# Performance work log

Hardware: AMD Instinct MI355X
Metric: run time of the kernel (lower is better)

The kernel has to match this reference:

```python
import jax, jax.numpy as jnp
import numpy as np
from jax import lax

NPOINT = 1024
RADIUS = 0.2
NSAMPLE = 32
MLP = (64, 64, 128)
BN_EPS = 1e-3  # keras BatchNormalization default epsilon


def setup_inputs() -> dict:
    key = jax.random.key(0)
    ks = jax.random.split(key, 8)
    B, N, C = 8, 8192, 64
    d = {
        'xyz': jax.random.uniform(ks[0], (B, N, 3), jnp.float32),
        'points': jax.random.normal(ks[1], (B, N, C), jnp.float32),
    }
    cin = C + 3  # use_xyz=True concatenates relative xyz
    for li, f in enumerate(MLP):
        d[f'w{li}'] = jax.random.normal(ks[2 + li], (cin, f), jnp.float32) * (1.0 / np.sqrt(cin))
        d[f'gamma{li}'] = jnp.ones((f,), jnp.float32)
        d[f'beta{li}'] = jnp.zeros((f,), jnp.float32)
        cin = f
    return d


def _fps(xyz, npoint):
    """Farthest point sampling. xyz: (B,N,3) -> (B,npoint) int32."""
    B, N, _ = xyz.shape

    def body(carry, _):
        dist, far = carry
        centroid = jnp.take_along_axis(xyz, far[:, None, None], axis=1)  # (B,1,3)
        d = jnp.sum((xyz - centroid) ** 2, axis=-1)  # (B,N)
        dist = jnp.minimum(dist, d)
        nxt = jnp.argmax(dist, axis=-1).astype(jnp.int32)
        return (dist, nxt), far

    init = (jnp.full((B, N), 1e10, xyz.dtype), jnp.zeros((B,), jnp.int32))
    _, idx = lax.scan(body, init, None, length=npoint)
    return jnp.transpose(idx)  # (B, npoint)


def _ball_query(xyz, new_xyz, radius, nsample):
    """xyz: (B,N,3), new_xyz: (B,S,3) -> (B,S,nsample) int32 neighbor idx."""
    B, S, _ = new_xyz.shape
    N = xyz.shape[1]
    sqr = jnp.sum((new_xyz[:, :, None, :] - xyz[:, None, :, :]) ** 2, axis=-1)  # (B,S,N)
    idx = jnp.broadcast_to(jnp.arange(N, dtype=jnp.int32), (B, S, N))
    idx = jnp.where(sqr > radius * radius, N, idx)
    idx = jnp.sort(idx, axis=-1)[:, :, :nsample]
    first = idx[:, :, :1]  # center itself is always in-radius -> valid
    return jnp.where(idx == N, first, idx)


def _gather(x, idx):
    """x: (B,N,C), idx: (B,S,K) -> (B,S,K,C)."""
    B, S, K = idx.shape
    flat = jnp.take_along_axis(x, idx.reshape(B, S * K)[:, :, None], axis=1)
    return flat.reshape(B, S, K, x.shape[-1])


def _bn_relu(x, gamma, beta):
    # training-mode batchnorm over (batch, npoint, nsample) axes
    m = jnp.mean(x, axis=(0, 1, 2), keepdims=True)
    v = jnp.var(x, axis=(0, 1, 2), keepdims=True)
    return jax.nn.relu(gamma * (x - m) * lax.rsqrt(v + BN_EPS) + beta)


def reference(xyz, points, w0, gamma0, beta0, w1, gamma1, beta1, w2, gamma2, beta2):
    fps_idx = _fps(xyz, NPOINT)  # (B,S)
    new_xyz = jnp.take_along_axis(xyz, fps_idx[:, :, None], axis=1)  # (B,S,3)
    idx = _ball_query(xyz, new_xyz, RADIUS, NSAMPLE)  # (B,S,K)
    grouped_xyz = _gather(xyz, idx) - new_xyz[:, :, None, :]  # (B,S,K,3)
    grouped_pts = _gather(points, idx)  # (B,S,K,C)
    x = jnp.concatenate([grouped_xyz, grouped_pts], axis=-1)  # (B,S,K,3+C)
    for w, g, b in ((w0, gamma0, beta0), (w1, gamma1, beta1), (w2, gamma2, beta2)):
        x = _bn_relu(jnp.einsum('bskc,cf->bskf', x, w), g, b)
    new_points = jnp.max(x, axis=2)  # (B,S,F) == squeeze of keepdims max
    return new_xyz, new_points
```

## Files before the change

### kernel.cpp

```cpp
#include <hip/hip_runtime.h>
#include <hip/hip_bf16.h>
#include <stdint.h>


#define INV_CNT (1.0f/262144.0f)

typedef __attribute__((ext_vector_type(8))) short bf16x8;
typedef __attribute__((ext_vector_type(4))) float f32x4;

__device__ __forceinline__ float bf2f(unsigned int v) {
    return __uint_as_float(v << 16);
}
__device__ __forceinline__ unsigned int f2bf(float f) {
    unsigned int u = __float_as_uint(f);
    return (u + 0x7fffu + ((u >> 16) & 1u)) >> 16;
}

template<int CTRL>
__device__ __forceinline__ unsigned int dpp_u32(unsigned int x) {
    return (unsigned int)__builtin_amdgcn_update_dpp((int)x, (int)x, CTRL, 0xf, 0xf, false);
}
template<int CTRL>
__device__ __forceinline__ float dpp_f32(float x) {
    return __uint_as_float(dpp_u32<CTRL>(__float_as_uint(x)));
}

__device__ __forceinline__ float2 fmin2(float2 a, float2 b) {
    return make_float2(fminf(a.x, b.x), fminf(a.y, b.y));
}
__device__ __forceinline__ float2 fmax2(float2 a, float2 b) {
    return make_float2(fmaxf(a.x, b.x), fmaxf(a.y, b.y));
}

__global__ __launch_bounds__(512) void fps_kernel(const float* __restrict__ xyz,
                                                  float* __restrict__ nxyz,
                                                  float* __restrict__ out_nxyz) {
#pragma clang fp contract(off)
    const int b = blockIdx.x;
    const int t = threadIdx.x;
    const int lane = t & 63;
    const int wv = t >> 6;
    const float* xb = xyz + (size_t)b * 8192 * 3;
    __shared__ float sx[8192], sy[8192], sz[8192];
    __shared__ unsigned long long sdk[2][8];
    __shared__ int ch[1024];
    float2 px[8], py[8], pz[8], dist[8];
#pragma unroll
    for (int j = 0; j < 8; ++j) {
        int p0 = t + (2*j)*512, p1 = t + (2*j+1)*512;
        float x0 = xb[p0*3+0], y0 = xb[p0*3+1], z0 = xb[p0*3+2];
        float x1 = xb[p1*3+0], y1 = xb[p1*3+1], z1 = xb[p1*3+2];
        px[j] = make_float2(x0, x1); py[j] = make_float2(y0, y1); pz[j] = make_float2(z0, z1);
        sx[p0] = x0; sy[p0] = y0; sz[p0] = z0;
        sx[p1] = x1; sy[p1] = y1; sz[p1] = z1;
        dist[j] = make_float2(1e10f, 1e10f);
    }
    __syncthreads();
    int far = 0;
    for (int it = 0; it < 1024; ++it) {
        if (t == 0) ch[it] = far;
        float cx = sx[far], cy = sy[far], cz = sz[far];
        float2 c2x = make_float2(cx, cx), c2y = make_float2(cy, cy), c2z = make_float2(cz, cz);
        float2 mx2 = make_float2(-1.f, -1.f);
#pragma unroll
        for (int j = 0; j < 8; ++j) {
            float2 dx = px[j] - c2x;
            float2 dy = py[j] - c2y;
            float2 dz = pz[j] - c2z;
            float2 d = (dx*dx + dy*dy) + dz*dz;
            float2 nd = fmin2(dist[j], d);
            dist[j] = nd;
            mx2 = fmax2(mx2, nd);
        }
        float v = fmaxf(mx2.x, mx2.y);
        v = fmaxf(v, dpp_f32<0x111>(v));
        v = fmaxf(v, dpp_f32<0x112>(v));
        v = fmaxf(v, dpp_f32<0x114>(v));
        v = fmaxf(v, dpp_f32<0x118>(v));
        v = fmaxf(v, dpp_f32<0x142>(v));
        v = fmaxf(v, dpp_f32<0x143>(v));
        float wm = __uint_as_float((unsigned int)__builtin_amdgcn_readlane((int)__float_as_uint(v), 63));
        unsigned int ci = 64u;
#pragma unroll
        for (int j = 7; j >= 0; --j) {
            if (dist[j].y == wm) ci = (unsigned int)(2*j+1);
            if (dist[j].x == wm) ci = (unsigned int)(2*j);
        }
        unsigned int idx = (ci == 64u) ? 0xffffffffu : (unsigned int)t + (ci << 9);
        { unsigned int n;
          n = dpp_u32<0x111>(idx); idx = (n < idx) ? n : idx;
          n = dpp_u32<0x112>(idx); idx = (n < idx) ? n : idx;
          n = dpp_u32<0x114>(idx); idx = (n < idx) ? n : idx;
          n = dpp_u32<0x118>(idx); idx = (n < idx) ? n : idx;
          n = dpp_u32<0x142>(idx); idx = (n < idx) ? n : idx;
          n = dpp_u32<0x143>(idx); idx = (n < idx) ? n : idx; }
        if (lane == 63)
            sdk[it & 1][wv] = ((unsigned long long)__float_as_uint(v) << 32)
                            | (unsigned long long)(~idx);
        __syncthreads();
        unsigned long long k = sdk[it & 1][lane & 7];
        unsigned int xh = (unsigned int)(k >> 32), xl = (unsigned int)k;
#define XSTEP(C) { unsigned int nh = dpp_u32<C>(xh), nl = dpp_u32<C>(xl);          \
                   unsigned long long nk = ((unsigned long long)nh << 32) | nl;     \
                   unsigned long long ck = ((unsigned long long)xh << 32) | xl;     \
                   bool tk = nk > ck; xh = tk ? nh : xh; xl = tk ? nl : xl; }
        XSTEP(0x111) XSTEP(0x112) XSTEP(0x114)
#undef XSTEP
        far = (int)(~(unsigned int)__builtin_amdgcn_readlane((int)xl, 7)) & 8191;
    }
    __syncthreads();
    for (int j = t; j < 1024; j += 512) {
        int ci = ch[j];
        float x = sx[ci], y = sy[ci], z = sz[ci];
        size_t o = (size_t)(b*1024 + j) * 3;
        nxyz[o] = x; nxyz[o+1] = y; nxyz[o+2] = z;
        out_nxyz[o] = x; out_nxyz[o+1] = y; out_nxyz[o+2] = z;
    }
}

__global__ __launch_bounds__(256) void ballquery_kernel(const float* __restrict__ xyz,
                                                        const float* __restrict__ nxyz,
                                                        int* __restrict__ idxbuf) {
    const int wib = threadIdx.x >> 6;
    const int lane = threadIdx.x & 63;
    const int c = blockIdx.x * 4 + wib;
    const int b = c >> 10;
    const float* xb = xyz + (size_t)b * 8192 * 3;
    const float cx = nxyz[c*3+0], cy = nxyz[c*3+1], cz = nxyz[c*3+2];
    const float R2 = 0.04f;
    int count = 0, first = 0;
    int* ob = idxbuf + (size_t)c * 32;
    for (int base = 0; base < 8192; base += 64) {
        int i = base + lane;
        float dx = __fsub_rn(xb[i*3+0], cx);
        float dy = __fsub_rn(xb[i*3+1], cy);
        float dz = __fsub_rn(xb[i*3+2], cz);
        float sq = __fadd_rn(__fadd_rn(__fmul_rn(dx,dx), __fmul_rn(dy,dy)), __fmul_rn(dz,dz));
        bool pass = !(sq > R2);
        unsigned long long mask = __ballot(pass);
        if (count == 0 && mask) first = base + (int)__builtin_ctzll(mask);
        int pos = count + (int)__popcll(mask & ((1ull << lane) - 1ull));
        if (pass && pos < 32) ob[pos] = i;
        count += (int)__popcll(mask);
        if (count >= 32) break;
    }
    if (count < 32 && lane >= count && lane < 32) ob[lane] = first;
}


__global__ __launch_bounds__(256) void layer0_kernel(
        const float* __restrict__ xyz, const float* __restrict__ points,
        const float* __restrict__ nxyz, const int* __restrict__ idxbuf,
        const float* __restrict__ w0, unsigned short* __restrict__ z0,
        float* __restrict__ stats0) {
    __shared__ __attribute__((aligned(16))) unsigned short Xb[64*104];
    __shared__ __attribute__((aligned(16))) unsigned short Wt[64*104];
    __shared__ float ssum[64], ssq[64];
    const int tid = threadIdx.x;
    const int R = blockIdx.x * 64;
    if (tid < 64) { ssum[tid] = 0.f; ssq[tid] = 0.f; }
    for (int i = tid; i < 67*64; i += 256) {
        int k = i >> 6, f = i & 63;
        Wt[f*104 + k] = (unsigned short)f2bf(w0[i]);
    }
    for (int i = tid; i < 29*64; i += 256) {
        int k = 67 + (i % 29), f = i / 29;
        Wt[f*104 + k] = 0;
    }
    {
        int r = tid >> 2, q = tid & 3;
        int row = R + r;
        int gi = idxbuf[row];
        int b = row >> 15, s = (row >> 5) & 1023;
        const float* pb = points + (size_t)(b*8192 + gi) * 64;
        int e0 = q*17, e1 = (q == 3) ? 67 : e0 + 17;
        for (int e = e0; e < e1; ++e) {
            float v;
            if (e < 3) v = xyz[(size_t)(b*8192+gi)*3 + e] - nxyz[(size_t)(b*1024+s)*3 + e];
            else       v = pb[e-3];
            Xb[r*104 + e] = (unsigned short)f2bf(v);
        }
    }
    for (int i = tid; i < 29*64; i += 256) {
        int e = 67 + (i % 29), r = i / 29;
        Xb[r*104 + e] = 0;
    }
    __syncthreads();
    const int l = tid & 63, w = tid >> 6;
    const int rsub = l & 15, kq = l >> 4;
    f32x4 acc[4];
#pragma unroll
    for (int cb = 0; cb < 4; ++cb) acc[cb] = (f32x4){0.f, 0.f, 0.f, 0.f};
    const int abase = (w*16 + rsub)*104 + kq*8;
    const int bbase = rsub*104 + kq*8;
#pragma unroll
    for (int ks = 0; ks < 3; ++ks) {
        bf16x8 A = *(const bf16x8*)&Xb[abase + ks*32];
#pragma unroll
        for (int cb = 0; cb < 4; ++cb) {
            bf16x8 Bf = *(const bf16x8*)&Wt[bbase + cb*16*104 + ks*32];
            acc[cb] = __builtin_amdgcn_mfma_f32_16x16x32_bf16(A, Bf, acc[cb], 0, 0, 0);
        }
    }
    unsigned short* zrow = z0 + (size_t)(R + w*16 + kq*4) * 64;
#pragma unroll
    for (int cb = 0; cb < 4; ++cb) {
        int c = cb*16 + rsub;
        float a0 = acc[cb][0], a1 = acc[cb][1], a2 = acc[cb][2], a3 = acc[cb][3];
        atomicAdd(&ssum[c], a0 + a1 + a2 + a3);
        atomicAdd(&ssq[c], a0*a0 + a1*a1 + a2*a2 + a3*a3);
#pragma unroll
        for (int j = 0; j < 4; ++j) zrow[j*64 + c] = (unsigned short)f2bf(acc[cb][j]);
    }
    __syncthreads();
    if (tid < 64) {
        atomicAdd(&stats0[tid], ssum[tid]);
        atomicAdd(&stats0[64+tid], ssq[tid]);
    }
}

__global__ __launch_bounds__(256) void layer1_kernel(
        const unsigned short* __restrict__ z0, const float* __restrict__ stats0,
        const float* __restrict__ gamma0, const float* __restrict__ beta0,
        const float* __restrict__ w1, unsigned short* __restrict__ z1,
        float* __restrict__ stats1) {
    __shared__ __attribute__((aligned(16))) unsigned short Xb[64*72];
    __shared__ __attribute__((aligned(16))) unsigned short Wt[64*72];
    __shared__ float scale[64], shift[64], ssum[64], ssq[64];
    const int tid = threadIdx.x;
    const int R = blockIdx.x * 64;
    if (tid < 64) {
        float m = stats0[tid] * INV_CNT;
        float v = stats0[64+tid] * INV_CNT - m*m;
        float rs = rsqrtf(v + 1e-3f);
        float sc = gamma0[tid] * rs;
        scale[tid] = sc; shift[tid] = beta0[tid] - m*sc;
        ssum[tid] = 0.f; ssq[tid] = 0.f;
    }
    for (int i = tid; i < 64*64; i += 256) {
        int k = i >> 6, f = i & 63;
        Wt[f*72 + k] = (unsigned short)f2bf(w1[i]);
    }
    __syncthreads();
    const uint4* zg = (const uint4*)(z0 + (size_t)R * 64);
#pragma unroll
    for (int cch = 0; cch < 2; ++cch) {
        int flat8 = tid*2 + cch;
        uint4 a = zg[flat8];
        int r = flat8 >> 3, e0 = (flat8 & 7) * 8;
        unsigned int uu[4] = {a.x, a.y, a.z, a.w};
        bf16x8 xv;
#pragma unroll
        for (int j = 0; j < 8; ++j) {
            unsigned int ub = (j & 1) ? (uu[j>>1] >> 16) : (uu[j>>1] & 0xffffu);
            float v = bf2f(ub);
            v = fmaxf(v * scale[e0+j] + shift[e0+j], 0.f);
            xv[j] = (short)f2bf(v);
        }
        *(bf16x8*)&Xb[r*72 + e0] = xv;
    }
    __syncthreads();
    const int l = tid & 63, w = tid >> 6;
    const int rsub = l & 15, kq = l >> 4;
    f32x4 acc[4];
#pragma unroll
    for (int cb = 0; cb < 4; ++cb) acc[cb] = (f32x4){0.f, 0.f, 0.f, 0.f};
    const int abase = (w*16 + rsub)*72 + kq*8;
    const int bbase = rsub*72 + kq*8;
#pragma unroll
    for (int ks = 0; ks < 2; ++ks) {
        bf16x8 A = *(const bf16x8*)&Xb[abase + ks*32];
#pragma unroll
        for (int cb = 0; cb < 4; ++cb) {
            bf16x8 Bf = *(const bf16x8*)&Wt[bbase + cb*16*72 + ks*32];
            acc[cb] = __builtin_amdgcn_mfma_f32_16x16x32_bf16(A, Bf, acc[cb], 0, 0, 0);
        }
    }
    unsigned short* zrow = z1 + (size_t)(R + w*16 + kq*4) * 64;
#pragma unroll
    for (int cb = 0; cb < 4; ++cb) {
        int c = cb*16 + rsub;
        float a0 = acc[cb][0], a1 = acc[cb][1], a2 = acc[cb][2], a3 = acc[cb][3];
        atomicAdd(&ssum[c], a0 + a1 + a2 + a3);
        atomicAdd(&ssq[c], a0*a0 + a1*a1 + a2*a2 + a3*a3);
#pragma unroll
        for (int j = 0; j < 4; ++j) zrow[j*64 + c] = (unsigned short)f2bf(acc[cb][j]);
    }
    __syncthreads();
    if (tid < 64) {
        atomicAdd(&stats1[tid], ssum[tid]);
        atomicAdd(&stats1[64+tid], ssq[tid]);
    }
}

__global__ __launch_bounds__(256) void layer2_kernel(
        const unsigned short* __restrict__ z1, const float* __restrict__ stats1,
        const float* __restrict__ gamma1, const float* __restrict__ beta1,
        const float* __restrict__ w2, float* __restrict__ maxz2,
        float* __restrict__ stats2) {
    __shared__ __attribute__((aligned(16))) unsigned short Xb[64*72];
    __shared__ __attribute__((aligned(16))) unsigned short Wt[128*72];
    __shared__ float scale[64], shift[64];
    __shared__ float ssum[128], ssq[128];
    __shared__ float gmx[2][8][128];
    const int tid = threadIdx.x;
    const int R = blockIdx.x * 64;
    if (tid < 64) {
        float m = stats1[tid] * INV_CNT;
        float v = stats1[64+tid] * INV_CNT - m*m;
        float rs = rsqrtf(v + 1e-3f);
        float sc = gamma1[tid] * rs;
        scale[tid] = sc; shift[tid] = beta1[tid] - m*sc;
    }
    if (tid < 128) { ssum[tid] = 0.f; ssq[tid] = 0.f; }
    for (int i = tid; i < 64*128; i += 256) {
        int k = i >> 7, f = i & 127;
        Wt[f*72 + k] = (unsigned short)f2bf(w2[i]);
    }
    __syncthreads();
    const uint4* zg = (const uint4*)(z1 + (size_t)R * 64);
#pragma unroll
    for (int cch = 0; cch < 2; ++cch) {
        int flat8 = tid*2 + cch;
        uint4 a = zg[flat8];
        int r = flat8 >> 3, e0 = (flat8 & 7) * 8;
        unsigned int uu[4] = {a.x, a.y, a.z, a.w};
        bf16x8 xv;
#pragma unroll
        for (int j = 0; j < 8; ++j) {
            unsigned int ub = (j & 1) ? (uu[j>>1] >> 16) : (uu[j>>1] & 0xffffu);
            float v = bf2f(ub);
            v = fmaxf(v * scale[e0+j] + shift[e0+j], 0.f);
            xv[j] = (short)f2bf(v);
        }
        *(bf16x8*)&Xb[r*72 + e0] = xv;
    }
    __syncthreads();
    const int l = tid & 63, w = tid >> 6;
    const int rsub = l & 15, kq = l >> 4;
    f32x4 acc[8];
#pragma unroll
    for (int cb = 0; cb < 8; ++cb) acc[cb] = (f32x4){0.f, 0.f, 0.f, 0.f};
    const int abase = (w*16 + rsub)*72 + kq*8;
    const int bbase = rsub*72 + kq*8;
#pragma unroll
    for (int ks = 0; ks < 2; ++ks) {
        bf16x8 A = *(const bf16x8*)&Xb[abase + ks*32];
#pragma unroll
        for (int cb = 0; cb < 8; ++cb) {
            bf16x8 Bf = *(const bf16x8*)&Wt[bbase + cb*16*72 + ks*32];
            acc[cb] = __builtin_amdgcn_mfma_f32_16x16x32_bf16(A, Bf, acc[cb], 0, 0, 0);
        }
    }
    const int g = w >> 1;
    const int contrib = (w & 1) * 4 + kq;
#pragma unroll
    for (int cb = 0; cb < 8; ++cb) {
        int c = cb*16 + rsub;
        float a0 = acc[cb][0], a1 = acc[cb][1], a2 = acc[cb][2], a3 = acc[cb][3];
        atomicAdd(&ssum[c], a0 + a1 + a2 + a3);
        atomicAdd(&ssq[c], a0*a0 + a1*a1 + a2*a2 + a3*a3);
        gmx[g][contrib][c] = fmaxf(fmaxf(a0, a1), fmaxf(a2, a3));
    }
    __syncthreads();
    {
        int gg = tid >> 7, c = tid & 127;
        float m = gmx[gg][0][c];
#pragma unroll
        for (int i = 1; i < 8; ++i) m = fmaxf(m, gmx[gg][i][c]);
        maxz2[(size_t)(blockIdx.x*2 + gg) * 128 + c] = m;
    }
    if (tid < 128) {
        atomicAdd(&stats2[tid], ssum[tid]);
        atomicAdd(&stats2[128+tid], ssq[tid]);
    }
}

__global__ __launch_bounds__(256) void final_kernel(
        const float* __restrict__ maxz2, const float* __restrict__ stats2,
        const float* __restrict__ gamma2, const float* __restrict__ beta2,
        float* __restrict__ out) {
    const int i = blockIdx.x * 256 + threadIdx.x;
    const int f = i & 127;
    float m = stats2[f] * INV_CNT;
    float v = stats2[128+f] * INV_CNT - m*m;
    float rs = rsqrtf(v + 1e-3f);
    out[24576 + i] = fmaxf(gamma2[f]*((maxz2[i]-m)*rs) + beta2[f], 0.f);
}

extern "C" void kernel_launch(void* const* d_in, const int* in_sizes, int n_in,
                              void* d_out, int out_size, void* d_ws, size_t ws_size,
                              hipStream_t stream) {
    const float* xyz    = (const float*)d_in[0];
    const float* points = (const float*)d_in[1];
    const float* w0     = (const float*)d_in[2];
    const float* g0     = (const float*)d_in[3];
    const float* b0     = (const float*)d_in[4];
    const float* w1     = (const float*)d_in[5];
    const float* g1     = (const float*)d_in[6];
    const float* b1     = (const float*)d_in[7];
    const float* w2     = (const float*)d_in[8];
    const float* g2     = (const float*)d_in[9];
    const float* b2     = (const float*)d_in[10];
    float* out = (float*)d_out;
    char* ws = (char*)d_ws;

    float* nxyz            = (float*)(ws + 0);
    int*   idxbuf          = (int*)  (ws + 98304);
    float* stats           = (float*)(ws + 1146880);
    unsigned short* z0     = (unsigned short*)(ws + 1148928);
    unsigned short* z1     = (unsigned short*)(ws + 34703360);
    float* maxz2           = (float*)(ws + 68257792);

    hipMemsetAsync(stats, 0, 512 * sizeof(float), stream);
    fps_kernel<<<8, 512, 0, stream>>>(xyz, nxyz, out);
    ballquery_kernel<<<2048, 256, 0, stream>>>(xyz, nxyz, idxbuf);
    layer0_kernel<<<4096, 256, 0, stream>>>(xyz, points, nxyz, idxbuf, w0, z0, stats);
    layer1_kernel<<<4096, 256, 0, stream>>>(z0, stats, g0, b0, w1, z1, stats + 128);
    layer2_kernel<<<4096, 256, 0, stream>>>(z1, stats + 128, g1, b1, w2, maxz2, stats + 256);
    final_kernel<<<4096, 256, 0, stream>>>(maxz2, stats + 256, g2, b2, out);
}
```

Before: 1.336 ms.

## Pack FPS distance math, gate argmax search, pre-convert weights, vectorize layer0 gather

FPS inner loop now uses packed f32 add/mul inline asm, and the per-lane index search runs only in lanes whose local max equals the wave max. Weight transposition and bf16 conversion move into a one-time prep kernel, so each layer block copies ready-made weights with 16-byte loads instead of converting per block. Layer0 gathers neighbor features with float4 loads. Together these cut the serial FPS critical path and redundant per-block work, at the cost of an extra launch and extra workspace.

```diff
diff --git a/kernel.cpp b/kernel.cpp
--- a/kernel.cpp
+++ b/kernel.cpp
@@ -7,6 +7,7 @@
 
 typedef __attribute__((ext_vector_type(8))) short bf16x8;
 typedef __attribute__((ext_vector_type(4))) float f32x4;
+typedef __attribute__((ext_vector_type(2))) float f32x2;
 
 __device__ __forceinline__ float bf2f(unsigned int v) {
     return __uint_as_float(v << 16);
@@ -25,11 +26,20 @@
     return __uint_as_float(dpp_u32<CTRL>(__float_as_uint(x)));
 }
 
-__device__ __forceinline__ float2 fmin2(float2 a, float2 b) {
-    return make_float2(fminf(a.x, b.x), fminf(a.y, b.y));
-}
-__device__ __forceinline__ float2 fmax2(float2 a, float2 b) {
-    return make_float2(fmaxf(a.x, b.x), fmaxf(a.y, b.y));
+__device__ __forceinline__ f32x2 pk_sub(f32x2 a, f32x2 b) {
+    f32x2 r;
+    asm("v_pk_add_f32 %0, %1, %2 neg_lo:[0,1] neg_hi:[0,1]" : "=v"(r) : "v"(a), "v"(b));
+    return r;
+}
+__device__ __forceinline__ f32x2 pk_sqr(f32x2 a) {
+    f32x2 r;
+    asm("v_pk_mul_f32 %0, %1, %1" : "=v"(r) : "v"(a));
+    return r;
+}
+__device__ __forceinline__ f32x2 pk_add(f32x2 a, f32x2 b) {
+    f32x2 r;
+    asm("v_pk_add_f32 %0, %1, %2" : "=v"(r) : "v"(a), "v"(b));
+    return r;
 }
 
 __global__ __launch_bounds__(512) void fps_kernel(const float* __restrict__ xyz,
@@ -44,49 +54,55 @@
     __shared__ float sx[8192], sy[8192], sz[8192];
     __shared__ unsigned long long sdk[2][8];
     __shared__ int ch[1024];
-    float2 px[8], py[8], pz[8], dist[8];
+    f32x2 px[8], py[8], pz[8], dist[8];
 #pragma unroll
     for (int j = 0; j < 8; ++j) {
         int p0 = t + (2*j)*512, p1 = t + (2*j+1)*512;
         float x0 = xb[p0*3+0], y0 = xb[p0*3+1], z0 = xb[p0*3+2];
         float x1 = xb[p1*3+0], y1 = xb[p1*3+1], z1 = xb[p1*3+2];
-        px[j] = make_float2(x0, x1); py[j] = make_float2(y0, y1); pz[j] = make_float2(z0, z1);
+        px[j] = (f32x2){x0, x1}; py[j] = (f32x2){y0, y1}; pz[j] = (f32x2){z0, z1};
         sx[p0] = x0; sy[p0] = y0; sz[p0] = z0;
         sx[p1] = x1; sy[p1] = y1; sz[p1] = z1;
-        dist[j] = make_float2(1e10f, 1e10f);
+        dist[j] = (f32x2){1e10f, 1e10f};
     }
     __syncthreads();
     int far = 0;
     for (int it = 0; it < 1024; ++it) {
         if (t == 0) ch[it] = far;
         float cx = sx[far], cy = sy[far], cz = sz[far];
-        float2 c2x = make_float2(cx, cx), c2y = make_float2(cy, cy), c2z = make_float2(cz, cz);
-        float2 mx2 = make_float2(-1.f, -1.f);
+        f32x2 c2x = (f32x2){cx, cx}, c2y = (f32x2){cy, cy}, c2z = (f32x2){cz, cz};
+        float bv0 = -1.f, bv1 = -1.f;
 #pragma unroll
         for (int j = 0; j < 8; ++j) {
-            float2 dx = px[j] - c2x;
-            float2 dy = py[j] - c2y;
-            float2 dz = pz[j] - c2z;
-            float2 d = (dx*dx + dy*dy) + dz*dz;
-            float2 nd = fmin2(dist[j], d);
-            dist[j] = nd;
-            mx2 = fmax2(mx2, nd);
-        }
-        float v = fmaxf(mx2.x, mx2.y);
+            f32x2 dx = pk_sub(px[j], c2x);
+            f32x2 dy = pk_sub(py[j], c2y);
+            f32x2 dz = pk_sub(pz[j], c2z);
+            f32x2 dd = pk_add(pk_add(pk_sqr(dx), pk_sqr(dy)), pk_sqr(dz));
+            float n0 = fminf(dist[j][0], dd[0]);
+            float n1 = fminf(dist[j][1], dd[1]);
+            dist[j][0] = n0; dist[j][1] = n1;
+            bv0 = fmaxf(bv0, n0); bv1 = fmaxf(bv1, n1);
+        }
+        float bestv = fmaxf(bv0, bv1);
+        float v = bestv;
         v = fmaxf(v, dpp_f32<0x111>(v));
         v = fmaxf(v, dpp_f32<0x112>(v));
         v = fmaxf(v, dpp_f32<0x114>(v));
         v = fmaxf(v, dpp_f32<0x118>(v));
         v = fmaxf(v, dpp_f32<0x142>(v));
         v = fmaxf(v, dpp_f32<0x143>(v));
-        float wm = __uint_as_float((unsigned int)__builtin_amdgcn_readlane((int)__float_as_uint(v), 63));
-        unsigned int ci = 64u;
-#pragma unroll
-        for (int j = 7; j >= 0; --j) {
-            if (dist[j].y == wm) ci = (unsigned int)(2*j+1);
-            if (dist[j].x == wm) ci = (unsigned int)(2*j);
-        }
-        unsigned int idx = (ci == 64u) ? 0xffffffffu : (unsigned int)t + (ci << 9);
+        unsigned int wmu = (unsigned int)__builtin_amdgcn_readlane((int)__float_as_uint(v), 63);
+        float wm = __uint_as_float(wmu);
+        unsigned int idx = 0xffffffffu;
+        if (bestv == wm) {
+            unsigned int ci = 0;
+#pragma unroll
+            for (int j = 7; j >= 0; --j) {
+                if (dist[j][1] == wm) ci = (unsigned int)(2*j+1);
+                if (dist[j][0] == wm) ci = (unsigned int)(2*j);
+            }
+            idx = (unsigned int)t + (ci << 9);
+        }
         { unsigned int n;
           n = dpp_u32<0x111>(idx); idx = (n < idx) ? n : idx;
           n = dpp_u32<0x112>(idx); idx = (n < idx) ? n : idx;
@@ -95,8 +111,7 @@
           n = dpp_u32<0x142>(idx); idx = (n < idx) ? n : idx;
           n = dpp_u32<0x143>(idx); idx = (n < idx) ? n : idx; }
         if (lane == 63)
-            sdk[it & 1][wv] = ((unsigned long long)__float_as_uint(v) << 32)
-                            | (unsigned long long)(~idx);
+            sdk[it & 1][wv] = ((unsigned long long)wmu << 32) | (unsigned long long)(~idx);
         __syncthreads();
         unsigned long long k = sdk[it & 1][lane & 7];
         unsigned int xh = (unsigned int)(k >> 32), xl = (unsigned int)k;
@@ -147,11 +162,33 @@
     if (count < 32 && lane >= count && lane < 32) ob[lane] = first;
 }
 
+__global__ __launch_bounds__(256) void prep_w(const float* __restrict__ w0,
+                                              const float* __restrict__ w1,
+                                              const float* __restrict__ w2,
+                                              unsigned short* __restrict__ wt0,
+                                              unsigned short* __restrict__ wt1,
+                                              unsigned short* __restrict__ wt2) {
+    const int i0 = blockIdx.x * 256 + threadIdx.x;
+    const int stride = gridDim.x * 256;
+    for (int i = i0; i < 64*104; i += stride) {
+        int f = i / 104, k = i - f*104;
+        wt0[i] = (k < 67) ? (unsigned short)f2bf(w0[k*64 + f]) : (unsigned short)0;
+    }
+    for (int i = i0; i < 64*72; i += stride) {
+        int f = i / 72, k = i - f*72;
+        wt1[i] = (k < 64) ? (unsigned short)f2bf(w1[k*64 + f]) : (unsigned short)0;
+    }
+    for (int i = i0; i < 128*72; i += stride) {
+        int f = i / 72, k = i - f*72;
+        wt2[i] = (k < 64) ? (unsigned short)f2bf(w2[k*128 + f]) : (unsigned short)0;
+    }
+}
+
 
 __global__ __launch_bounds__(256) void layer0_kernel(
         const float* __restrict__ xyz, const float* __restrict__ points,
         const float* __restrict__ nxyz, const int* __restrict__ idxbuf,
-        const float* __restrict__ w0, unsigned short* __restrict__ z0,
+        const unsigned short* __restrict__ wt0, unsigned short* __restrict__ z0,
         float* __restrict__ stats0) {
     __shared__ __attribute__((aligned(16))) unsigned short Xb[64*104];
     __shared__ __attribute__((aligned(16))) unsigned short Wt[64*104];
@@ -159,26 +196,33 @@
     const int tid = threadIdx.x;
     const int R = blockIdx.x * 64;
     if (tid < 64) { ssum[tid] = 0.f; ssq[tid] = 0.f; }
-    for (int i = tid; i < 67*64; i += 256) {
-        int k = i >> 6, f = i & 63;
-        Wt[f*104 + k] = (unsigned short)f2bf(w0[i]);
-    }
-    for (int i = tid; i < 29*64; i += 256) {
-        int k = 67 + (i % 29), f = i / 29;
-        Wt[f*104 + k] = 0;
+    {
+        const uint4* src = (const uint4*)wt0;
+        uint4* dst = (uint4*)Wt;
+        for (int i = tid; i < 64*104/8; i += 256) dst[i] = src[i];
     }
     {
         int r = tid >> 2, q = tid & 3;
         int row = R + r;
         int gi = idxbuf[row];
         int b = row >> 15, s = (row >> 5) & 1023;
-        const float* pb = points + (size_t)(b*8192 + gi) * 64;
-        int e0 = q*17, e1 = (q == 3) ? 67 : e0 + 17;
-        for (int e = e0; e < e1; ++e) {
-            float v;
-            if (e < 3) v = xyz[(size_t)(b*8192+gi)*3 + e] - nxyz[(size_t)(b*1024+s)*3 + e];
-            else       v = pb[e-3];
-            Xb[r*104 + e] = (unsigned short)f2bf(v);
+        const float4* pb4 = (const float4*)(points + (size_t)(b*8192 + gi) * 64);
+        float4 f0 = pb4[q*4+0], f1 = pb4[q*4+1], f2 = pb4[q*4+2], f3 = pb4[q*4+3];
+        unsigned short* xr = &Xb[r*104 + 3 + q*16];
+        xr[0]  = (unsigned short)f2bf(f0.x); xr[1]  = (unsigned short)f2bf(f0.y);
+        xr[2]  = (unsigned short)f2bf(f0.z); xr[3]  = (unsigned short)f2bf(f0.w);
+        xr[4]  = (unsigned short)f2bf(f1.x); xr[5]  = (unsigned short)f2bf(f1.y);
+        xr[6]  = (unsigned short)f2bf(f1.z); xr[7]  = (unsigned short)f2bf(f1.w);
+        xr[8]  = (unsigned short)f2bf(f2.x); xr[9]  = (unsigned short)f2bf(f2.y);
+        xr[10] = (unsigned short)f2bf(f2.z); xr[11] = (unsigned short)f2bf(f2.w);
+        xr[12] = (unsigned short)f2bf(f3.x); xr[13] = (unsigned short)f2bf(f3.y);
+        xr[14] = (unsigned short)f2bf(f3.z); xr[15] = (unsigned short)f2bf(f3.w);
+        if (q == 0) {
+#pragma unroll
+            for (int e = 0; e < 3; ++e) {
+                float vv = xyz[(size_t)(b*8192+gi)*3 + e] - nxyz[(size_t)(b*1024+s)*3 + e];
+                Xb[r*104 + e] = (unsigned short)f2bf(vv);
+            }
         }
     }
     for (int i = tid; i < 29*64; i += 256) {
@@ -222,7 +266,7 @@
 __global__ __launch_bounds__(256) void layer1_kernel(
         const unsigned short* __restrict__ z0, const float* __restrict__ stats0,
         const float* __restrict__ gamma0, const float* __restrict__ beta0,
-        const float* __restrict__ w1, unsigned short* __restrict__ z1,
+        const unsigned short* __restrict__ wt1, unsigned short* __restrict__ z1,
         float* __restrict__ stats1) {
     __shared__ __attribute__((aligned(16))) unsigned short Xb[64*72];
     __shared__ __attribute__((aligned(16))) unsigned short Wt[64*72];
@@ -237,9 +281,10 @@
         scale[tid] = sc; shift[tid] = beta0[tid] - m*sc;
         ssum[tid] = 0.f; ssq[tid] = 0.f;
     }
-    for (int i = tid; i < 64*64; i += 256) {
-        int k = i >> 6, f = i & 63;
-        Wt[f*72 + k] = (unsigned short)f2bf(w1[i]);
+    {
+        const uint4* src = (const uint4*)wt1;
+        uint4* dst = (uint4*)Wt;
+        for (int i = tid; i < 64*72/8; i += 256) dst[i] = src[i];
     }
     __syncthreads();
     const uint4* zg = (const uint4*)(z0 + (size_t)R * 64);
@@ -296,7 +341,7 @@
 __global__ __launch_bounds__(256) void layer2_kernel(
         const unsigned short* __restrict__ z1, const float* __restrict__ stats1,
         const float* __restrict__ gamma1, const float* __restrict__ beta1,
-        const float* __restrict__ w2, float* __restrict__ maxz2,
+        const unsigned short* __restrict__ wt2, float* __restrict__ maxz2,
         float* __restrict__ stats2) {
     __shared__ __attribute__((aligned(16))) unsigned short Xb[64*72];
     __shared__ __attribute__((aligned(16))) unsigned short Wt[128*72];
@@ -313,9 +358,10 @@
         scale[tid] = sc; shift[tid] = beta1[tid] - m*sc;
     }
     if (tid < 128) { ssum[tid] = 0.f; ssq[tid] = 0.f; }
-    for (int i = tid; i < 64*128; i += 256) {
-        int k = i >> 7, f = i & 127;
-        Wt[f*72 + k] = (unsigned short)f2bf(w2[i]);
+    {
+        const uint4* src = (const uint4*)wt2;
+        uint4* dst = (uint4*)Wt;
+        for (int i = tid; i < 128*72/8; i += 256) dst[i] = src[i];
     }
     __syncthreads();
     const uint4* zg = (const uint4*)(z1 + (size_t)R * 64);
@@ -411,12 +457,16 @@
     unsigned short* z0     = (unsigned short*)(ws + 1148928);
     unsigned short* z1     = (unsigned short*)(ws + 34703360);
     float* maxz2           = (float*)(ws + 68257792);
+    unsigned short* wt0    = (unsigned short*)(ws + 72452096);
+    unsigned short* wt1    = (unsigned short*)(ws + 72465408);
+    unsigned short* wt2    = (unsigned short*)(ws + 72474624);
 
     hipMemsetAsync(stats, 0, 512 * sizeof(float), stream);
+    prep_w<<<26, 256, 0, stream>>>(w0, w1, w2, wt0, wt1, wt2);
     fps_kernel<<<8, 512, 0, stream>>>(xyz, nxyz, out);
     ballquery_kernel<<<2048, 256, 0, stream>>>(xyz, nxyz, idxbuf);
-    layer0_kernel<<<4096, 256, 0, stream>>>(xyz, points, nxyz, idxbuf, w0, z0, stats);
-    layer1_kernel<<<4096, 256, 0, stream>>>(z0, stats, g0, b0, w1, z1, stats + 128);
-    layer2_kernel<<<4096, 256, 0, stream>>>(z1, stats + 128, g1, b1, w2, maxz2, stats + 256);
+    layer0_kernel<<<4096, 256, 0, stream>>>(xyz, points, nxyz, idxbuf, wt0, z0, stats);
+    layer1_kernel<<<4096, 256, 0, stream>>>(z0, stats, g0, b0, wt1, z1, stats + 128);
+    layer2_kernel<<<4096, 256, 0, stream>>>(z1, stats + 128, g1, b1, wt2, maxz2, stats + 256);
     final_kernel<<<4096, 256, 0, stream>>>(maxz2, stats + 256, g2, b2, out);
 }
```

Measured after the change: 1.567 ms. +17.2%, slower.
